# Performance work log

Hardware: AMD Instinct MI355X
Metric: run time of the kernel (lower is better)

The kernel has to match this reference:

```python
import jax, jax.numpy as jnp
import numpy as np

B, NQ, NK = 4, 2048, 2048
CQ, CK = 1024, 768
H = 16
D = CQ // H  # 64
EPS = 1e-5


def layernorm(x, gamma, beta):
    mu = jnp.mean(x, axis=-1, keepdims=True)
    var = jnp.var(x, axis=-1, keepdims=True)
    return (x - mu) * jax.lax.rsqrt(var + EPS) * gamma + beta


def setup_inputs() -> dict:
    key = jax.random.key(0)
    ks = jax.random.split(key, 12)
    s_q = 1.0 / np.sqrt(CQ)
    s_c = 1.0 / np.sqrt(CK)
    return {
        "query_tokens": jax.random.normal(ks[0], (B, NQ, CQ), jnp.float32),
        "context_tokens": jax.random.normal(ks[1], (B, NK, CK), jnp.float32),
        "Wq": jax.random.uniform(ks[2], (CQ, CQ), jnp.float32, -s_q, s_q),
        "bq": jnp.zeros((CQ,), jnp.float32),
        "Wk": jax.random.uniform(ks[3], (CK, CQ), jnp.float32, -s_c, s_c),
        "bk": jnp.zeros((CQ,), jnp.float32),
        "Wv": jax.random.uniform(ks[4], (CK, CQ), jnp.float32, -s_c, s_c),
        "bv": jnp.zeros((CQ,), jnp.float32),
        "Wo": jax.random.uniform(ks[5], (CQ, CQ), jnp.float32, -s_q, s_q),
        "bo": jnp.zeros((CQ,), jnp.float32),
        "gamma_q": jnp.ones((CQ,), jnp.float32),
        "beta_q": jnp.zeros((CQ,), jnp.float32),
        "gamma_ctx": jnp.ones((CK,), jnp.float32),
        "beta_ctx": jnp.zeros((CK,), jnp.float32),
    }


def reference(query_tokens, context_tokens, Wq, bq, Wk, bk, Wv, bv, Wo, bo,
              gamma_q, beta_q, gamma_ctx, beta_ctx):
    scale = 1.0 / np.sqrt(D)
    xq = layernorm(query_tokens, gamma_q, beta_q)      # [B,NQ,CQ]
    xc = layernorm(context_tokens, gamma_ctx, beta_ctx)  # [B,NK,CK]
    q = (xq @ Wq + bq).reshape(B, NQ, H, D)
    k = (xc @ Wk + bk).reshape(B, NK, H, D)
    v = (xc @ Wv + bv).reshape(B, NK, H, D)
    scores = jnp.einsum('bqhd,bkhd->bhqk', q, k) * scale  # [B,H,NQ,NK]
    attn = jax.nn.softmax(scores, axis=-1)
    attended = jnp.einsum('bhqk,bkhd->bqhd', attn, v).reshape(B, NQ, CQ)
    return attended @ Wo + bo
```

## Files before the change

kernel.cpp:

```cpp
#include <hip/hip_runtime.h>
#include <hip/hip_bf16.h>
#include <stdint.h>

#define B_    4
#define NQ_   2048
#define NK_   2048
#define CQ_   1024
#define CK_   768
#define H_    16
#define D_    64
#define SCALE 0.125f
#define C2    0.1803368801111204f

typedef __attribute__((ext_vector_type(8))) short bf16x8;
typedef __attribute__((ext_vector_type(4))) float f32x4;

#define MFMA16(a, b, c) __builtin_amdgcn_mfma_f32_16x16x32_bf16((a), (b), (c), 0, 0, 0)

#define GLL16(gp, lp)                                                                 \
    __builtin_amdgcn_global_load_lds(                                                 \
        (__attribute__((address_space(1))) uint32_t*)(uintptr_t)(gp),                 \
        (__attribute__((address_space(3))) uint32_t*)(uintptr_t)(lp), 16, 0, 0)

__device__ inline unsigned short f2bf(float f) {
    union { float f; uint32_t u; } v; v.f = f;
    uint32_t u = v.u;
    return (unsigned short)((u + 0x7fffu + ((u >> 16) & 1u)) >> 16);
}

__device__ inline uint32_t packbf2(float a, float b) {
    union { __hip_bfloat162 h; uint32_t u; } v;
    v.h = __float22bfloat162_rn(float2{a, b});
    return v.u;
}

template <int W>
__global__ __launch_bounds__(256) void ln_bf16(const float* __restrict__ x,
                                               const float* __restrict__ gamma,
                                               const float* __restrict__ beta,
                                               unsigned short* __restrict__ out) {
    int row = blockIdx.x;
    int tid = threadIdx.x;
    int col = tid * 4;
    const float* xr = x + (size_t)row * W;
    float v0 = 0.f, v1 = 0.f, v2 = 0.f, v3 = 0.f;
    float s = 0.f, s2 = 0.f;
    bool active = (col < W);
    if (active) {
        float4 vv = *(const float4*)(xr + col);
        v0 = vv.x; v1 = vv.y; v2 = vv.z; v3 = vv.w;
        s = v0 + v1 + v2 + v3;
        s2 = v0 * v0 + v1 * v1 + v2 * v2 + v3 * v3;
    }
    for (int off = 32; off >= 1; off >>= 1) {
        s += __shfl_xor(s, off);
        s2 += __shfl_xor(s2, off);
    }
    __shared__ float red[8];
    __shared__ float stat[2];
    int wid = tid >> 6, lane = tid & 63;
    if (lane == 0) { red[wid] = s; red[4 + wid] = s2; }
    __syncthreads();
    if (tid == 0) {
        float ts = red[0] + red[1] + red[2] + red[3];
        float ts2 = red[4] + red[5] + red[6] + red[7];
        float mu = ts / (float)W;
        float var = ts2 / (float)W - mu * mu;
        stat[0] = mu;
        stat[1] = rsqrtf(var + 1e-5f);
    }
    __syncthreads();
    float mu = stat[0], rstd = stat[1];
    if (active) {
        float4 g = *(const float4*)(gamma + col);
        float4 b = *(const float4*)(beta + col);
        ushort4 o;
        o.x = f2bf((v0 - mu) * rstd * g.x + b.x);
        o.y = f2bf((v1 - mu) * rstd * g.y + b.y);
        o.z = f2bf((v2 - mu) * rstd * g.z + b.z);
        o.w = f2bf((v3 - mu) * rstd * g.w + b.w);
        *(ushort4*)(out + (size_t)row * W + col) = o;
    }
}

__global__ __launch_bounds__(256) void transpose_cast(const float* __restrict__ Wsrc,
                                                      unsigned short* __restrict__ Wt,
                                                      int K, int N) {
    __shared__ float t[32][33];
    int n0 = blockIdx.x * 32, k0 = blockIdx.y * 32;
    int tx = threadIdx.x, ty = threadIdx.y;
    for (int i = 0; i < 4; i++)
        t[ty + 8 * i][tx] = Wsrc[(size_t)(k0 + ty + 8 * i) * N + n0 + tx];
    __syncthreads();
    for (int i = 0; i < 4; i++)
        Wt[(size_t)(n0 + ty + 8 * i) * K + k0 + tx] = f2bf(t[tx][ty + 8 * i]);
}

template <int MODE>
__global__ __launch_bounds__(256) void gemm_bt(const unsigned short* __restrict__ X,
                                               const unsigned short* __restrict__ Wt,
                                               const float* __restrict__ bias,
                                               void* __restrict__ outp, int Kd) {
    __shared__ __align__(16) unsigned short As[128 * 64];
    __shared__ __align__(16) unsigned short Bs[128 * 64];
    int tid = threadIdx.x;
    int lane = tid & 63, wid = tid >> 6;

    int lin = blockIdx.y * 8 + blockIdx.x;
    int virt = (lin & 7) * 64 + (lin >> 3);
    int m0 = (virt >> 3) * 128;
    int n0 = (virt & 7) * 128;
    int wm = wid >> 1, wn = wid & 1;

    f32x4 acc[4][4];
    for (int i = 0; i < 4; i++)
        for (int j = 0; j < 4; j++) acc[i][j] = (f32x4){0.f, 0.f, 0.f, 0.f};

    int srow = wid * 8 + (lane >> 3);
    int sxor = ((lane & 7) * 16) ^ (((lane >> 3) & 7) << 4);
    int swz = (lane & 7) << 4;
    const char* Xb = (const char*)X;
    const char* Wb = (const char*)Wt;
    char* AsB = (char*)As;
    char* BsB = (char*)Bs;

    for (int k0 = 0; k0 < Kd; k0 += 64) {
        for (int i = 0; i < 4; i++) {
            int row = i * 32 + srow;
            GLL16(Xb + ((size_t)(m0 + row) * Kd + k0) * 2 + sxor, AsB + i * 4096 + wid * 1024);
            GLL16(Wb + ((size_t)(n0 + row) * Kd + k0) * 2 + sxor, BsB + i * 4096 + wid * 1024);
        }
        __syncthreads();
        for (int kk = 0; kk < 2; kk++) {
            int cb = (((lane >> 4) * 16 + kk * 64) ^ swz);
            bf16x8 a[4], b[4];
            for (int mf = 0; mf < 4; mf++)
                a[mf] = *(const bf16x8*)(AsB + (wm * 64 + mf * 16 + (lane & 15)) * 128 + cb);
            for (int nf = 0; nf < 4; nf++)
                b[nf] = *(const bf16x8*)(BsB + (wn * 64 + nf * 16 + (lane & 15)) * 128 + cb);
            for (int mf = 0; mf < 4; mf++)
                for (int nf = 0; nf < 4; nf++) acc[mf][nf] = MFMA16(a[mf], b[nf], acc[mf][nf]);
        }
        __syncthreads();
    }

    int crow0 = m0 + wm * 64;
    int ccol0 = n0 + wn * 64;
    for (int nf = 0; nf < 4; nf++) {
        int col = ccol0 + nf * 16 + (lane & 15);
        float bv = bias[col];
        for (int mf = 0; mf < 4; mf++) {
            int rowb = crow0 + mf * 16 + (lane >> 4) * 4;
            for (int r = 0; r < 4; r++) {
                int row = rowb + r;
                float val = acc[mf][nf][r] + bv;
                if (MODE == 2) {
                    ((float*)outp)[(size_t)row * 1024 + col] = val;
                } else {
                    int b = row >> 11, nq = row & 2047;
                    int h = col >> 6, d = col & 63;
                    unsigned short bfv = f2bf(val);
                    if (MODE == 0)
                        ((unsigned short*)outp)[(((size_t)(b * H_ + h)) * NQ_ + nq) * 64 + d] = bfv;
                    else
                        ((unsigned short*)outp)[(((size_t)(b * H_ + h)) * 64 + d) * NK_ + nq] = bfv;
                }
            }
        }
    }
}

__global__ __launch_bounds__(512, 4) void flash_attn(const unsigned short* __restrict__ Q,
                                                     const unsigned short* __restrict__ K,
                                                     const unsigned short* __restrict__ Vt,
                                                     unsigned short* __restrict__ attended) {
    __shared__ __align__(16) char smem[2][16384];
    __shared__ __align__(16) unsigned short Ps[8][2048];
    int tid = threadIdx.x, lane = tid & 63, wid = tid >> 6;
    int g = lane >> 4;
    int q = lane & 15;

    int lin = blockIdx.y * 8 + blockIdx.x;
    int virt = (lin & 7) * 64 + (lin >> 3);
    int bh = virt >> 3;
    int q0 = (virt & 7) * 256;
    const char* Qb = (const char*)(Q + (size_t)bh * NQ_ * 64);
    const char* Kb = (const char*)(K + (size_t)bh * NK_ * 64);
    const char* Vb = (const char*)(Vt + (size_t)bh * 64 * NK_);

    int qrow = q0 + wid * 32 + q;
    bf16x8 qf0[2], qf1[2];
    qf0[0] = *(const bf16x8*)(Qb + (size_t)qrow * 128 + g * 16);
    qf0[1] = *(const bf16x8*)(Qb + (size_t)qrow * 128 + g * 16 + 64);
    qf1[0] = *(const bf16x8*)(Qb + (size_t)(qrow + 16) * 128 + g * 16);
    qf1[1] = *(const bf16x8*)(Qb + (size_t)(qrow + 16) * 128 + g * 16 + 64);

    bf16x8 onesf;
#pragma unroll
    for (int i = 0; i < 8; i++) onesf[i] = (short)0x3f80;

    f32x4 acc0[4], acc1[4];
    for (int i = 0; i < 4; i++) {
        acc0[i] = (f32x4){0.f, 0.f, 0.f, 0.f};
        acc1[i] = (f32x4){0.f, 0.f, 0.f, 0.f};
    }
    f32x4 accl0 = (f32x4){0.f, 0.f, 0.f, 0.f};
    f32x4 accl1 = (f32x4){0.f, 0.f, 0.f, 0.f};
    float mst = -3.0e38f;

    int sxor = ((lane & 7) * 16) ^ (((lane >> 3) & 7) << 4);
    const char* kptr = Kb + (size_t)(wid * 8 + (lane >> 3)) * 128 + sxor;
    const char* vptr = Vb + (size_t)(wid * 8 + (lane >> 3)) * 4096 + sxor;
    int cb0 = g * 16;
    int swz = (lane & 7) << 4;

    unsigned short* Pw = Ps[wid];
    uint32_t* P32 = (uint32_t*)Pw;
    int pwbase = q * 32 + ((g & 1) << 1);
    int q7 = q & 7;

    GLL16(kptr, smem[0] + wid * 1024);
    GLL16(vptr, smem[0] + 8192 + wid * 1024);
    kptr += 8192;
    vptr += 128;
    __syncthreads();
    int cur = 0;

    for (int t = 0; t < NK_ / 64; ++t) {
        if (t < NK_ / 64 - 1) {
            GLL16(kptr, smem[cur ^ 1] + wid * 1024);
            GLL16(vptr, smem[cur ^ 1] + 8192 + wid * 1024);
            kptr += 8192;
            vptr += 128;
        }
        const char* Ksb = smem[cur];
        const char* Vsb = smem[cur] + 8192;

        f32x4 s0[4], s1[4];
        __builtin_amdgcn_s_setprio(1);
#pragma unroll
        for (int nf = 0; nf < 4; nf++) {
            s0[nf] = (f32x4){0.f, 0.f, 0.f, 0.f};
            s1[nf] = (f32x4){0.f, 0.f, 0.f, 0.f};
#pragma unroll
            for (int kk = 0; kk < 2; kk++) {
                bf16x8 kf = *(const bf16x8*)(Ksb + (nf * 16 + q) * 128 + ((cb0 + kk * 64) ^ swz));
                s0[nf] = MFMA16(kf, qf0[kk], s0[nf]);
                s1[nf] = MFMA16(kf, qf1[kk], s1[nf]);
            }
        }
        __builtin_amdgcn_s_setprio(0);

#define VMAX4(a, b) (f32x4){fmaxf(a[0], b[0]), fmaxf(a[1], b[1]), fmaxf(a[2], b[2]), fmaxf(a[3], b[3])}
        f32x4 x0 = VMAX4(s0[0], s1[0]);
        f32x4 x1 = VMAX4(s0[1], s1[1]);
        f32x4 x2 = VMAX4(s0[2], s1[2]);
        f32x4 x3 = VMAX4(s0[3], s1[3]);
        x0 = VMAX4(x0, x2);
        x1 = VMAX4(x1, x3);
        x0 = VMAX4(x0, x1);
        float mloc = fmaxf(fmaxf(x0[0], x0[1]), fmaxf(x0[2], x0[3]));
        mloc = fmaxf(mloc, __shfl_xor(mloc, 16));
        mloc = fmaxf(mloc, __shfl_xor(mloc, 32));

        if (!__all(mloc - mst <= 44.36f)) {
            float mnew = fmaxf(mst, mloc);
            float alpha = __builtin_amdgcn_exp2f((mst - mnew) * C2);
            mst = mnew;
            float al[4];
#pragma unroll
            for (int r = 0; r < 4; r++) al[r] = __shfl(alpha, 4 * g + r);
#pragma unroll
            for (int r = 0; r < 4; r++) {
#pragma unroll
                for (int df = 0; df < 4; df++) {
                    acc0[df][r] *= al[r];
                    acc1[df][r] *= al[r];
                }
                accl0[r] *= al[r];
                accl1[r] *= al[r];
            }
        }

        float mc = mst * C2;
#pragma unroll
        for (int nf = 0; nf < 4; nf++) {
            int idx = pwbase + (((2 * nf + (g >> 1)) ^ q7) << 2);
            {
                float e0 = __builtin_amdgcn_exp2f(s0[nf][0] * C2 - mc);
                float e1 = __builtin_amdgcn_exp2f(s0[nf][1] * C2 - mc);
                float e2 = __builtin_amdgcn_exp2f(s0[nf][2] * C2 - mc);
                float e3 = __builtin_amdgcn_exp2f(s0[nf][3] * C2 - mc);
                P32[idx] = packbf2(e0, e1);
                P32[idx + 1] = packbf2(e2, e3);
            }
            {
                float e0 = __builtin_amdgcn_exp2f(s1[nf][0] * C2 - mc);
                float e1 = __builtin_amdgcn_exp2f(s1[nf][1] * C2 - mc);
                float e2 = __builtin_amdgcn_exp2f(s1[nf][2] * C2 - mc);
                float e3 = __builtin_amdgcn_exp2f(s1[nf][3] * C2 - mc);
                P32[idx + 512] = packbf2(e0, e1);
                P32[idx + 513] = packbf2(e2, e3);
            }
        }

        __builtin_amdgcn_s_setprio(1);
#pragma unroll
        for (int kk = 0; kk < 2; kk++) {
            int pb = q * 128 + (((g + 4 * kk) ^ q7) << 4);
            bf16x8 ap0 = *(const bf16x8*)((const char*)Pw + pb);
            bf16x8 ap1 = *(const bf16x8*)((const char*)Pw + 2048 + pb);
            accl0 = MFMA16(ap0, onesf, accl0);
            accl1 = MFMA16(ap1, onesf, accl1);
#pragma unroll
            for (int df = 0; df < 4; df++) {
                bf16x8 bv = *(const bf16x8*)(Vsb + (df * 16 + q) * 128 + ((cb0 + kk * 64) ^ swz));
                acc0[df] = MFMA16(ap0, bv, acc0[df]);
                acc1[df] = MFMA16(ap1, bv, acc1[df]);
            }
        }
        __builtin_amdgcn_s_setprio(0);
        __syncthreads();
        cur ^= 1;
    }

    int b = bh >> 4, h = bh & 15;
#pragma unroll
    for (int df = 0; df < 4; df++)
#pragma unroll
        for (int r = 0; r < 4; r++) {
            int row = q0 + wid * 32 + 4 * g + r;
            int col = h * 64 + df * 16 + q;
            attended[(size_t)(b * NQ_ + row) * CQ_ + col] = f2bf(acc0[df][r] / accl0[r]);
            attended[(size_t)(b * NQ_ + row + 16) * CQ_ + col] = f2bf(acc1[df][r] / accl1[r]);
        }
}

extern "C" void kernel_launch(void* const* d_in, const int* in_sizes, int n_in,
                              void* d_out, int out_size, void* d_ws, size_t ws_size,
                              hipStream_t stream) {
    const float* qt  = (const float*)d_in[0];
    const float* ct  = (const float*)d_in[1];
    const float* Wq  = (const float*)d_in[2];
    const float* bq  = (const float*)d_in[3];
    const float* Wk  = (const float*)d_in[4];
    const float* bk  = (const float*)d_in[5];
    const float* Wv  = (const float*)d_in[6];
    const float* bv  = (const float*)d_in[7];
    const float* Wo  = (const float*)d_in[8];
    const float* bo  = (const float*)d_in[9];
    const float* gq  = (const float*)d_in[10];
    const float* btq = (const float*)d_in[11];
    const float* gc  = (const float*)d_in[12];
    const float* btc = (const float*)d_in[13];

    char* ws = (char*)d_ws;
    unsigned short* xq  = (unsigned short*)(ws + 0);
    unsigned short* xc  = (unsigned short*)(ws + 16777216);
    unsigned short* Wqt = (unsigned short*)(ws + 29360128);
    unsigned short* Wkt = (unsigned short*)(ws + 31457280);
    unsigned short* Wvt = (unsigned short*)(ws + 33030144);
    unsigned short* Wot = (unsigned short*)(ws + 34603008);
    unsigned short* Qb  = (unsigned short*)(ws + 36700160);
    unsigned short* Kb  = (unsigned short*)(ws + 53477376);
    unsigned short* Vtb = (unsigned short*)(ws + 70254592);

    ln_bf16<1024><<<8192, 256, 0, stream>>>(qt, gq, btq, xq);
    ln_bf16<768><<<8192, 256, 0, stream>>>(ct, gc, btc, xc);

    transpose_cast<<<dim3(32, 32), dim3(32, 8), 0, stream>>>(Wq, Wqt, 1024, 1024);
    transpose_cast<<<dim3(32, 24), dim3(32, 8), 0, stream>>>(Wk, Wkt, 768, 1024);
    transpose_cast<<<dim3(32, 24), dim3(32, 8), 0, stream>>>(Wv, Wvt, 768, 1024);
    transpose_cast<<<dim3(32, 32), dim3(32, 8), 0, stream>>>(Wo, Wot, 1024, 1024);

    gemm_bt<0><<<dim3(8, 64), 256, 0, stream>>>(xq, Wqt, bq, Qb, 1024);
    gemm_bt<0><<<dim3(8, 64), 256, 0, stream>>>(xc, Wkt, bk, Kb, 768);
    gemm_bt<1><<<dim3(8, 64), 256, 0, stream>>>(xc, Wvt, bv, Vtb, 768);

    flash_attn<<<dim3(8, 64), 512, 0, stream>>>(Qb, Kb, Vtb, xq);

    gemm_bt<2><<<dim3(8, 64), 256, 0, stream>>>(xq, Wot, bo, d_out, 1024);
}
```

Before: 209.9 us.

## Fuse launches: merged layernorm, transposes, K/V GEMM; restructure attention softmax/PV

The two layernorm launches become one kernel and the four weight transposes become one kernel. The K and V projections become a single GEMM over a concatenated 2048-column weight, so the context activations are read once. In flash attention, K fragments are loaded once per tile and reused for both query halves, and the exp/PV stages for the two halves are split so one half's exp work can overlap the other's MFMA. This cuts launch count and duplicate loads, at the cost of more register pressure in the attention loop.

```diff
diff --git a/kernel.cpp b/kernel.cpp
--- a/kernel.cpp
+++ b/kernel.cpp
@@ -34,20 +34,34 @@
     return v.u;
 }
 
-template <int W>
-__global__ __launch_bounds__(256) void ln_bf16(const float* __restrict__ x,
-                                               const float* __restrict__ gamma,
-                                               const float* __restrict__ beta,
-                                               unsigned short* __restrict__ out) {
+__global__ __launch_bounds__(256) void ln_fused(const float* __restrict__ xqt,
+                                                const float* __restrict__ xct,
+                                                const float* __restrict__ gq,
+                                                const float* __restrict__ btq,
+                                                const float* __restrict__ gc,
+                                                const float* __restrict__ btc,
+                                                unsigned short* __restrict__ oq,
+                                                unsigned short* __restrict__ oc) {
     int row = blockIdx.x;
+    const float *x, *gamma, *beta;
+    unsigned short* out;
+    int W;
+    float invW;
+    if (row < 8192) {
+        x = xqt + (size_t)row * 1024; gamma = gq; beta = btq;
+        out = oq + (size_t)row * 1024; W = 1024; invW = 1.f / 1024.f;
+    } else {
+        int r = row - 8192;
+        x = xct + (size_t)r * 768; gamma = gc; beta = btc;
+        out = oc + (size_t)r * 768; W = 768; invW = 1.f / 768.f;
+    }
     int tid = threadIdx.x;
     int col = tid * 4;
-    const float* xr = x + (size_t)row * W;
     float v0 = 0.f, v1 = 0.f, v2 = 0.f, v3 = 0.f;
     float s = 0.f, s2 = 0.f;
     bool active = (col < W);
     if (active) {
-        float4 vv = *(const float4*)(xr + col);
+        float4 vv = *(const float4*)(x + col);
         v0 = vv.x; v1 = vv.y; v2 = vv.z; v3 = vv.w;
         s = v0 + v1 + v2 + v3;
         s2 = v0 * v0 + v1 * v1 + v2 * v2 + v3 * v3;
@@ -64,8 +78,8 @@
     if (tid == 0) {
         float ts = red[0] + red[1] + red[2] + red[3];
         float ts2 = red[4] + red[5] + red[6] + red[7];
-        float mu = ts / (float)W;
-        float var = ts2 / (float)W - mu * mu;
+        float mu = ts * invW;
+        float var = ts2 * invW - mu * mu;
         stat[0] = mu;
         stat[1] = rsqrtf(var + 1e-5f);
     }
@@ -79,37 +93,52 @@
         o.y = f2bf((v1 - mu) * rstd * g.y + b.y);
         o.z = f2bf((v2 - mu) * rstd * g.z + b.z);
         o.w = f2bf((v3 - mu) * rstd * g.w + b.w);
-        *(ushort4*)(out + (size_t)row * W + col) = o;
-    }
-}
-
-__global__ __launch_bounds__(256) void transpose_cast(const float* __restrict__ Wsrc,
-                                                      unsigned short* __restrict__ Wt,
-                                                      int K, int N) {
+        *(ushort4*)(out + col) = o;
+    }
+}
+
+__global__ __launch_bounds__(256) void transpose_all(const float* __restrict__ Wq,
+                                                     const float* __restrict__ Wk,
+                                                     const float* __restrict__ Wv,
+                                                     const float* __restrict__ Wo,
+                                                     unsigned short* __restrict__ Wqt,
+                                                     unsigned short* __restrict__ Wkvt,
+                                                     unsigned short* __restrict__ Wot) {
     __shared__ float t[32][33];
-    int n0 = blockIdx.x * 32, k0 = blockIdx.y * 32;
+    int blk = blockIdx.x;
+    const float* src;
+    unsigned short* dst;
+    int K;
+    if (blk < 1024)      { src = Wq; dst = Wqt; K = 1024; }
+    else if (blk < 1792) { blk -= 1024; src = Wk; dst = Wkvt; K = 768; }
+    else if (blk < 2560) { blk -= 1792; src = Wv; dst = Wkvt + (size_t)1024 * 768; K = 768; }
+    else                 { blk -= 2560; src = Wo; dst = Wot; K = 1024; }
+    int n0 = (blk & 31) * 32, k0 = (blk >> 5) * 32;
     int tx = threadIdx.x, ty = threadIdx.y;
     for (int i = 0; i < 4; i++)
-        t[ty + 8 * i][tx] = Wsrc[(size_t)(k0 + ty + 8 * i) * N + n0 + tx];
+        t[ty + 8 * i][tx] = src[(size_t)(k0 + ty + 8 * i) * 1024 + n0 + tx];
     __syncthreads();
     for (int i = 0; i < 4; i++)
-        Wt[(size_t)(n0 + ty + 8 * i) * K + k0 + tx] = f2bf(t[tx][ty + 8 * i]);
+        dst[(size_t)(n0 + ty + 8 * i) * K + k0 + tx] = f2bf(t[tx][ty + 8 * i]);
 }
 
 template <int MODE>
 __global__ __launch_bounds__(256) void gemm_bt(const unsigned short* __restrict__ X,
                                                const unsigned short* __restrict__ Wt,
-                                               const float* __restrict__ bias,
-                                               void* __restrict__ outp, int Kd) {
+                                               const float* __restrict__ bias0,
+                                               const float* __restrict__ bias1,
+                                               void* __restrict__ out0,
+                                               void* __restrict__ out1, int Kd) {
+    constexpr int NB = (MODE == 3) ? 16 : 8;
     __shared__ __align__(16) unsigned short As[128 * 64];
     __shared__ __align__(16) unsigned short Bs[128 * 64];
     int tid = threadIdx.x;
     int lane = tid & 63, wid = tid >> 6;
 
-    int lin = blockIdx.y * 8 + blockIdx.x;
-    int virt = (lin & 7) * 64 + (lin >> 3);
-    int m0 = (virt >> 3) * 128;
-    int n0 = (virt & 7) * 128;
+    int lin = blockIdx.y * NB + blockIdx.x;
+    int virt = (lin & 7) * (NB * 8) + (lin >> 3);
+    int m0 = (virt / NB) * 128;
+    int n0 = (virt % NB) * 128;
     int wm = wid >> 1, wn = wid & 1;
 
     f32x4 acc[4][4];
@@ -148,22 +177,34 @@
     int ccol0 = n0 + wn * 64;
     for (int nf = 0; nf < 4; nf++) {
         int col = ccol0 + nf * 16 + (lane & 15);
-        float bv = bias[col];
+        float bv_;
+        if (MODE == 3)
+            bv_ = (col < 1024) ? bias0[col] : bias1[col - 1024];
+        else
+            bv_ = bias0[col];
         for (int mf = 0; mf < 4; mf++) {
             int rowb = crow0 + mf * 16 + (lane >> 4) * 4;
             for (int r = 0; r < 4; r++) {
                 int row = rowb + r;
-                float val = acc[mf][nf][r] + bv;
+                float val = acc[mf][nf][r] + bv_;
                 if (MODE == 2) {
-                    ((float*)outp)[(size_t)row * 1024 + col] = val;
+                    ((float*)out0)[(size_t)row * 1024 + col] = val;
                 } else {
                     int b = row >> 11, nq = row & 2047;
-                    int h = col >> 6, d = col & 63;
                     unsigned short bfv = f2bf(val);
-                    if (MODE == 0)
-                        ((unsigned short*)outp)[(((size_t)(b * H_ + h)) * NQ_ + nq) * 64 + d] = bfv;
-                    else
-                        ((unsigned short*)outp)[(((size_t)(b * H_ + h)) * 64 + d) * NK_ + nq] = bfv;
+                    if (MODE == 0) {
+                        int h = col >> 6, d = col & 63;
+                        ((unsigned short*)out0)[(((size_t)(b * H_ + h)) * NQ_ + nq) * 64 + d] = bfv;
+                    } else {
+                        if (col < 1024) {
+                            int h = col >> 6, d = col & 63;
+                            ((unsigned short*)out0)[(((size_t)(b * H_ + h)) * NQ_ + nq) * 64 + d] = bfv;
+                        } else {
+                            int c = col - 1024;
+                            int h = c >> 6, d = c & 63;
+                            ((unsigned short*)out1)[(((size_t)(b * H_ + h)) * 64 + d) * NK_ + nq] = bfv;
+                        }
+                    }
                 }
             }
         }
@@ -218,6 +259,11 @@
     uint32_t* P32 = (uint32_t*)Pw;
     int pwbase = q * 32 + ((g & 1) << 1);
     int q7 = q & 7;
+    int pidx[4], prb[2];
+#pragma unroll
+    for (int nf = 0; nf < 4; nf++) pidx[nf] = pwbase + (((2 * nf + (g >> 1)) ^ q7) << 2);
+#pragma unroll
+    for (int kk = 0; kk < 2; kk++) prb[kk] = q * 128 + (((g + 4 * kk) ^ q7) << 4);
 
     GLL16(kptr, smem[0] + wid * 1024);
     GLL16(vptr, smem[0] + 8192 + wid * 1024);
@@ -236,18 +282,26 @@
         const char* Ksb = smem[cur];
         const char* Vsb = smem[cur] + 8192;
 
+        bf16x8 kf[4][2];
+#pragma unroll
+        for (int nf = 0; nf < 4; nf++)
+#pragma unroll
+            for (int kk = 0; kk < 2; kk++)
+                kf[nf][kk] = *(const bf16x8*)(Ksb + (nf * 16 + q) * 128 + ((cb0 + kk * 64) ^ swz));
+
         f32x4 s0[4], s1[4];
         __builtin_amdgcn_s_setprio(1);
 #pragma unroll
         for (int nf = 0; nf < 4; nf++) {
             s0[nf] = (f32x4){0.f, 0.f, 0.f, 0.f};
+            s0[nf] = MFMA16(kf[nf][0], qf0[0], s0[nf]);
+            s0[nf] = MFMA16(kf[nf][1], qf0[1], s0[nf]);
+        }
+#pragma unroll
+        for (int nf = 0; nf < 4; nf++) {
             s1[nf] = (f32x4){0.f, 0.f, 0.f, 0.f};
-#pragma unroll
-            for (int kk = 0; kk < 2; kk++) {
-                bf16x8 kf = *(const bf16x8*)(Ksb + (nf * 16 + q) * 128 + ((cb0 + kk * 64) ^ swz));
-                s0[nf] = MFMA16(kf, qf0[kk], s0[nf]);
-                s1[nf] = MFMA16(kf, qf1[kk], s1[nf]);
-            }
+            s1[nf] = MFMA16(kf[nf][0], qf1[0], s1[nf]);
+            s1[nf] = MFMA16(kf[nf][1], qf1[1], s1[nf]);
         }
         __builtin_amdgcn_s_setprio(0);
 
@@ -281,43 +335,49 @@
                 accl1[r] *= al[r];
             }
         }
-
         float mc = mst * C2;
+
 #pragma unroll
         for (int nf = 0; nf < 4; nf++) {
-            int idx = pwbase + (((2 * nf + (g >> 1)) ^ q7) << 2);
-            {
-                float e0 = __builtin_amdgcn_exp2f(s0[nf][0] * C2 - mc);
-                float e1 = __builtin_amdgcn_exp2f(s0[nf][1] * C2 - mc);
-                float e2 = __builtin_amdgcn_exp2f(s0[nf][2] * C2 - mc);
-                float e3 = __builtin_amdgcn_exp2f(s0[nf][3] * C2 - mc);
-                P32[idx] = packbf2(e0, e1);
-                P32[idx + 1] = packbf2(e2, e3);
-            }
-            {
-                float e0 = __builtin_amdgcn_exp2f(s1[nf][0] * C2 - mc);
-                float e1 = __builtin_amdgcn_exp2f(s1[nf][1] * C2 - mc);
-                float e2 = __builtin_amdgcn_exp2f(s1[nf][2] * C2 - mc);
-                float e3 = __builtin_amdgcn_exp2f(s1[nf][3] * C2 - mc);
-                P32[idx + 512] = packbf2(e0, e1);
-                P32[idx + 513] = packbf2(e2, e3);
-            }
-        }
-
+            float e0 = __builtin_amdgcn_exp2f(s0[nf][0] * C2 - mc);
+            float e1 = __builtin_amdgcn_exp2f(s0[nf][1] * C2 - mc);
+            float e2 = __builtin_amdgcn_exp2f(s0[nf][2] * C2 - mc);
+            float e3 = __builtin_amdgcn_exp2f(s0[nf][3] * C2 - mc);
+            P32[pidx[nf]] = packbf2(e0, e1);
+            P32[pidx[nf] + 1] = packbf2(e2, e3);
+        }
         __builtin_amdgcn_s_setprio(1);
 #pragma unroll
         for (int kk = 0; kk < 2; kk++) {
-            int pb = q * 128 + (((g + 4 * kk) ^ q7) << 4);
-            bf16x8 ap0 = *(const bf16x8*)((const char*)Pw + pb);
-            bf16x8 ap1 = *(const bf16x8*)((const char*)Pw + 2048 + pb);
-            accl0 = MFMA16(ap0, onesf, accl0);
-            accl1 = MFMA16(ap1, onesf, accl1);
+            bf16x8 ap0 = *(const bf16x8*)((const char*)Pw + prb[kk]);
 #pragma unroll
             for (int df = 0; df < 4; df++) {
                 bf16x8 bv = *(const bf16x8*)(Vsb + (df * 16 + q) * 128 + ((cb0 + kk * 64) ^ swz));
                 acc0[df] = MFMA16(ap0, bv, acc0[df]);
+            }
+            accl0 = MFMA16(ap0, onesf, accl0);
+        }
+        __builtin_amdgcn_s_setprio(0);
+
+#pragma unroll
+        for (int nf = 0; nf < 4; nf++) {
+            float e0 = __builtin_amdgcn_exp2f(s1[nf][0] * C2 - mc);
+            float e1 = __builtin_amdgcn_exp2f(s1[nf][1] * C2 - mc);
+            float e2 = __builtin_amdgcn_exp2f(s1[nf][2] * C2 - mc);
+            float e3 = __builtin_amdgcn_exp2f(s1[nf][3] * C2 - mc);
+            P32[pidx[nf] + 512] = packbf2(e0, e1);
+            P32[pidx[nf] + 513] = packbf2(e2, e3);
+        }
+        __builtin_amdgcn_s_setprio(1);
+#pragma unroll
+        for (int kk = 0; kk < 2; kk++) {
+            bf16x8 ap1 = *(const bf16x8*)((const char*)Pw + 2048 + prb[kk]);
+#pragma unroll
+            for (int df = 0; df < 4; df++) {
+                bf16x8 bv = *(const bf16x8*)(Vsb + (df * 16 + q) * 128 + ((cb0 + kk * 64) ^ swz));
                 acc1[df] = MFMA16(ap1, bv, acc1[df]);
             }
+            accl1 = MFMA16(ap1, onesf, accl1);
         }
         __builtin_amdgcn_s_setprio(0);
         __syncthreads();
@@ -355,29 +415,22 @@
     const float* btc = (const float*)d_in[13];
 
     char* ws = (char*)d_ws;
-    unsigned short* xq  = (unsigned short*)(ws + 0);
-    unsigned short* xc  = (unsigned short*)(ws + 16777216);
-    unsigned short* Wqt = (unsigned short*)(ws + 29360128);
-    unsigned short* Wkt = (unsigned short*)(ws + 31457280);
-    unsigned short* Wvt = (unsigned short*)(ws + 33030144);
-    unsigned short* Wot = (unsigned short*)(ws + 34603008);
-    unsigned short* Qb  = (unsigned short*)(ws + 36700160);
-    unsigned short* Kb  = (unsigned short*)(ws + 53477376);
-    unsigned short* Vtb = (unsigned short*)(ws + 70254592);
-
-    ln_bf16<1024><<<8192, 256, 0, stream>>>(qt, gq, btq, xq);
-    ln_bf16<768><<<8192, 256, 0, stream>>>(ct, gc, btc, xc);
-
-    transpose_cast<<<dim3(32, 32), dim3(32, 8), 0, stream>>>(Wq, Wqt, 1024, 1024);
-    transpose_cast<<<dim3(32, 24), dim3(32, 8), 0, stream>>>(Wk, Wkt, 768, 1024);
-    transpose_cast<<<dim3(32, 24), dim3(32, 8), 0, stream>>>(Wv, Wvt, 768, 1024);
-    transpose_cast<<<dim3(32, 32), dim3(32, 8), 0, stream>>>(Wo, Wot, 1024, 1024);
-
-    gemm_bt<0><<<dim3(8, 64), 256, 0, stream>>>(xq, Wqt, bq, Qb, 1024);
-    gemm_bt<0><<<dim3(8, 64), 256, 0, stream>>>(xc, Wkt, bk, Kb, 768);
-    gemm_bt<1><<<dim3(8, 64), 256, 0, stream>>>(xc, Wvt, bv, Vtb, 768);
+    unsigned short* xq   = (unsigned short*)(ws + 0);
+    unsigned short* xc   = (unsigned short*)(ws + 16777216);
+    unsigned short* Wqt  = (unsigned short*)(ws + 29360128);
+    unsigned short* Wkvt = (unsigned short*)(ws + 31457280);
+    unsigned short* Wot  = (unsigned short*)(ws + 34603008);
+    unsigned short* Qb   = (unsigned short*)(ws + 36700160);
+    unsigned short* Kb   = (unsigned short*)(ws + 53477376);
+    unsigned short* Vtb  = (unsigned short*)(ws + 70254592);
+
+    ln_fused<<<16384, 256, 0, stream>>>(qt, ct, gq, btq, gc, btc, xq, xc);
+    transpose_all<<<3584, dim3(32, 8), 0, stream>>>(Wq, Wk, Wv, Wo, Wqt, Wkvt, Wot);
+
+    gemm_bt<0><<<dim3(8, 64), 256, 0, stream>>>(xq, Wqt, bq, nullptr, Qb, nullptr, 1024);
+    gemm_bt<3><<<dim3(16, 64), 256, 0, stream>>>(xc, Wkvt, bk, bv, Kb, Vtb, 768);
 
     flash_attn<<<dim3(8, 64), 512, 0, stream>>>(Qb, Kb, Vtb, xq);
 
-    gemm_bt<2><<<dim3(8, 64), 256, 0, stream>>>(xq, Wot, bo, d_out, 1024);
-}
+    gemm_bt<2><<<dim3(8, 64), 256, 0, stream>>>(xq, Wot, bo, nullptr, d_out, nullptr, 1024);
+}
```

New measurement: 217.5 us. +3.6%, slower.
